# Kernel optimization log

Hardware: AMD Instinct MI355X
Metric: run time of the kernel (lower is better)

## Reference

```python
import jax, jax.numpy as jnp
import numpy as np

# Config (matches init_kwargs)
N_PARTS = 4
N_DATASETS = 2
N_VOLUMES = 16
N_TRANSFORMS = 2
TEMP_FAC = 0.1
BS = N_PARTS * N_DATASETS * N_VOLUMES          # 128
N_TOTAL = BS * (N_TRANSFORMS + 1)              # 384 rows in reg_pred
D_FEAT = 131072
PD = N_PARTS * N_DATASETS                      # class period for denominator exclusion
EPS = 1e-6


def setup_inputs() -> dict:
    key = jax.random.key(0)
    reg_pred = jax.random.normal(key, (N_TOTAL, D_FEAT), dtype=jnp.float32)
    return {"reg_pred": reg_pred}


def reference(reg_pred) -> jnp.ndarray:
    # Cosine similarity with torch's eps clamp on each norm.
    norms = jnp.maximum(jnp.linalg.norm(reg_pred, axis=1, keepdims=True), EPS)
    xn = reg_pred / norms                                   # [N, D]
    sims = (xn @ xn.T) / TEMP_FAC                           # [N, N] full cos-sim matrix
    e = jnp.exp(sims)

    # Denominator for pos_index p excludes every column j with j % PD == p % PD
    # (dataset_similar=False, within_dataset=False). Precompute per-class column sums.
    jmod = jnp.arange(N_TOTAL) % PD                          # [N]
    class_sum = jax.ops.segment_sum(e.T, jmod, num_segments=PD).T  # [N, PD]
    row_sum = jnp.sum(e, axis=1)                             # [N]

    p = jnp.arange(BS)
    rem = p % PD
    i1 = p
    i2 = BS + p
    i3 = (p + PD) % N_TOTAL
    i4 = (BS + p + PD) % N_TOTAL
    i5 = 2 * BS + p
    i6 = (2 * BS + p + PD) % N_TOTAL

    def pair_loss(a, b):
        en = e[a, b]                                         # exp(cos(xi,xj)/t), [BS]
        den_a = row_sum[a] - class_sum[a, rem]               # sum exp over den indexes
        den_b = row_sum[b] - class_sum[b, rem]
        return jnp.sum(-jnp.log(en / (en + den_a)) - jnp.log(en / (en + den_b)))

    total = (pair_loss(i1, i2) + pair_loss(i3, i4) + pair_loss(i1, i3)
             + pair_loss(i2, i4) + pair_loss(i5, i6) + pair_loss(i2, i5)
             + pair_loss(i4, i6))
    return total / (N_TRANSFORMS * 3 * BS)
```

## Files before the change

kernel.cpp:

```cpp
#include <hip/hip_runtime.h>
#include <hip/hip_bf16.h>

#define N_TOTAL 384
#define BS 128
#define PD 8
#define D_FEAT 131072
#define EPS 1e-6f

#define NSTRIP 256
#define COLS_PER (D_FEAT / NSTRIP)
#define CHUNK 64
#define NCH (COLS_PER / CHUNK)
#define NSWEEP 12
#define NSLOT 24

typedef __attribute__((ext_vector_type(4))) float f32x4;
typedef __attribute__((ext_vector_type(8))) __bf16 bf16x8;
typedef __attribute__((ext_vector_type(4))) __bf16 bf16x4;

typedef __attribute__((address_space(1))) const unsigned int gu32;
typedef __attribute__((address_space(3))) unsigned int lu32;

__device__ __forceinline__ void gload16(const void* g, void* l) {
    __builtin_amdgcn_global_load_lds((gu32*)g, (lu32*)l, 16, 0, 0);
}

static __device__ const int SAt[8][3] = {{0,0,0},{0,0,0},{1,1,1},{1,1,1},
                                         {2,2,4},{2,2,4},{3,3,5},{3,3,5}};
static __device__ const int SBt[8][3] = {{0,1,2},{3,4,5},{0,1,2},{3,4,5},
                                         {2,3,4},{4,5,5},{2,3,4},{4,5,5}};
static __device__ const int SRB2[NSLOT] = {0,0,0, 0,0,0, 1,1,1, 1,1,1,
                                           2,2,4, 2,2,4, 3,3,5, 3,3,5};
static __device__ const int SCB2[NSLOT] = {0,1,2, 3,4,5, 0,1,2, 3,4,5,
                                           2,3,4, 4,5,5, 2,3,4, 4,5,5};

__device__ __forceinline__ float gsym(const float* __restrict__ G, int i, int j) {
    return ((i >> 7) <= (j >> 7)) ? G[(size_t)i * N_TOTAL + j]
                                  : G[(size_t)j * N_TOTAL + i];
}

__device__ __forceinline__ bf16x8 fragb(const char* smb, int row, int ks, int kg) {
    return *(const bf16x8*)(smb + row * 128 + ((((ks << 2) | kg) ^ (row & 7)) << 4));
}

__global__ __launch_bounds__(512) void gram_fused_kernel(const float* __restrict__ X,
                                                         __bf16* __restrict__ P) {
    __shared__ char smf[N_TOTAL * 256];
    __shared__ char smb[N_TOTAL * 128];

    const int strip = blockIdx.x;
    const int tid  = threadIdx.x;
    const int wave = tid >> 6;
    const int lane = tid & 63;
    const int r16  = lane & 15;
    const int kg   = lane >> 4;

    const int A0 = SAt[wave][0] * 64, A2 = SAt[wave][2] * 64;
    const int B0 = SBt[wave][0] * 64, B1 = SBt[wave][1] * 64, B2 = SBt[wave][2] * 64;

    const char* src0 = (const char*)X + (size_t)(tid >> 4) * (D_FEAT * 4)
                     + (size_t)strip * (COLS_PER * 4) + (tid & 15) * 16;

    const int cr   = tid >> 4;
    const int g16  = tid & 15;
    const int wswz = ((((g16 >> 1) ^ (cr & 7)) << 4) | ((g16 & 1) << 3));

    f32x4 acc0[4][4], acc1[4][4], acc2[4][4];
#pragma unroll
    for (int m = 0; m < 4; m++)
#pragma unroll
        for (int n = 0; n < 4; n++) {
            acc0[m][n] = (f32x4)(0.0f); acc1[m][n] = (f32x4)(0.0f); acc2[m][n] = (f32x4)(0.0f);
        }

#define STAGE(t)                                                                          \
    _Pragma("unroll") for (int s = 0; s < NSWEEP; s++)                                    \
        gload16(src0 + (size_t)s * (32ull * D_FEAT * 4) + (size_t)(t) * 256,              \
                smf + s * 8192 + tid * 16);

#define SUBT(accX, Bb, ks)                                                                \
    do {                                                                                  \
        bf16x8 bf[4];                                                                     \
        _Pragma("unroll") for (int n = 0; n < 4; n++)                                     \
            bf[n] = fragb(smb, (Bb) + n * 16 + r16, ks, kg);                              \
        _Pragma("unroll") for (int m = 0; m < 4; m++)                                     \
            _Pragma("unroll") for (int n = 0; n < 4; n++)                                 \
                accX[m][n] = __builtin_amdgcn_mfma_f32_16x16x32_bf16(af[m], bf[n],        \
                                                                     accX[m][n], 0, 0, 0);\
    } while (0)

    STAGE(0);

    for (int t = 0; t < NCH; ++t) {
        asm volatile("s_waitcnt vmcnt(0)" ::: "memory");
        __builtin_amdgcn_sched_barrier(0);
        __builtin_amdgcn_s_barrier();
        __builtin_amdgcn_sched_barrier(0);

#pragma unroll
        for (int s = 0; s < NSWEEP; s++) {
            const f32x4 v = *(const f32x4*)(smf + s * 8192 + tid * 16);
            bf16x4 o;
            o[0] = (__bf16)v[0]; o[1] = (__bf16)v[1];
            o[2] = (__bf16)v[2]; o[3] = (__bf16)v[3];
            *(bf16x4*)(smb + (s * 32 + cr) * 128 + wswz) = o;
        }

        asm volatile("s_waitcnt lgkmcnt(0)" ::: "memory");
        __builtin_amdgcn_sched_barrier(0);
        __builtin_amdgcn_s_barrier();
        __builtin_amdgcn_sched_barrier(0);
        if (t + 1 < NCH) STAGE(t + 1);

#pragma unroll
        for (int ks = 0; ks < 2; ++ks) {
            bf16x8 af[4];
#pragma unroll
            for (int m = 0; m < 4; m++) af[m] = fragb(smb, A0 + m * 16 + r16, ks, kg);
            SUBT(acc0, B0, ks);
            SUBT(acc1, B1, ks);
#pragma unroll
            for (int m = 0; m < 4; m++) af[m] = fragb(smb, A2 + m * 16 + r16, ks, kg);
            SUBT(acc2, B2, ks);
        }
    }
#undef STAGE
#undef SUBT

    const int crow = (lane >> 4) * 4;
    const int ccol = lane & 15;
#define STOREP(accX, s)                                                                   \
    do {                                                                                  \
        __bf16* base = P + ((size_t)strip * NSLOT + wave * 3 + (s)) * 4096;               \
        _Pragma("unroll") for (int m = 0; m < 4; m++)                                     \
            _Pragma("unroll") for (int n = 0; n < 4; n++) {                               \
                bf16x4 v;                                                                 \
                v[0] = (__bf16)accX[m][n][0]; v[1] = (__bf16)accX[m][n][1];               \
                v[2] = (__bf16)accX[m][n][2]; v[3] = (__bf16)accX[m][n][3];               \
                *(bf16x4*)(base + (n * 16 + ccol) * 64 + m * 16 + crow) = v;              \
            }                                                                             \
    } while (0)
    STOREP(acc0, 0);
    STOREP(acc1, 1);
    STOREP(acc2, 2);
#undef STOREP
}

__global__ __launch_bounds__(128) void reduce_kernel(const __bf16* __restrict__ P,
                                                     float* __restrict__ G) {
    const int gidx = blockIdx.x * 128 + threadIdx.x;
    const int slot = gidx >> 11;
    const int pe   = (gidx & 2047) * 2;

    const unsigned* p = (const unsigned*)(P + (size_t)slot * 4096 + pe);
    const size_t stride = (size_t)NSLOT * 4096 / 2;
    float s0 = 0.0f, s1 = 0.0f;
#pragma unroll 16
    for (int strip = 0; strip < NSTRIP; ++strip) {
        const unsigned u = p[stride * strip];
        s0 += __uint_as_float(u << 16);
        s1 += __uint_as_float(u & 0xffff0000u);
    }

    const int rb  = SRB2[slot] * 64;
    const int cb  = SCB2[slot] * 64;
    const int col = pe >> 6;
    const int row = pe & 63;
    G[(size_t)(rb + row)     * N_TOTAL + cb + col] = s0;
    G[(size_t)(rb + row + 1) * N_TOTAL + cb + col] = s1;
}

__global__ __launch_bounds__(128) void den_kernel(const float* __restrict__ G,
                                                  float* __restrict__ den) {
    const int i = blockIdx.x;
    __shared__ float sInv[N_TOTAL];
    for (int j = threadIdx.x; j < N_TOTAL; j += 128) {
        const float n = sqrtf(G[(size_t)j * N_TOTAL + j]);
        sInv[j] = 1.0f / fmaxf(n, EPS);
    }
    __syncthreads();

    const float mi  = sInv[i] * 10.0f;
    const int   myc = i & 7;
    float s = 0.0f;
    for (int j = threadIdx.x; j < N_TOTAL; j += 128) {
        if ((j & 7) != myc)
            s += expf(gsym(G, i, j) * mi * sInv[j]);
    }
#pragma unroll
    for (int off = 32; off > 0; off >>= 1) s += __shfl_down(s, off, 64);
    __shared__ float partial[2];
    if ((threadIdx.x & 63) == 0) partial[threadIdx.x >> 6] = s;
    __syncthreads();
    if (threadIdx.x == 0) den[i] = partial[0] + partial[1];
}

__global__ __launch_bounds__(256) void loss_kernel(const float* __restrict__ G,
                                                   const float* __restrict__ den,
                                                   float* __restrict__ out) {
    __shared__ float sInv[N_TOTAL];
    for (int j = threadIdx.x; j < N_TOTAL; j += 256) {
        const float n = sqrtf(G[(size_t)j * N_TOTAL + j]);
        sInv[j] = 1.0f / fmaxf(n, EPS);
    }
    __syncthreads();

    float s = 0.0f;
    for (int idx = threadIdx.x; idx < 7 * BS; idx += 256) {
        const int p   = idx & (BS - 1);
        const int set = idx >> 7;
        int a, b;
        switch (set) {
            case 0:  a = p;                        b = BS + p;                      break;
            case 1:  a = (p + PD) % N_TOTAL;       b = (BS + p + PD) % N_TOTAL;     break;
            case 2:  a = p;                        b = (p + PD) % N_TOTAL;          break;
            case 3:  a = BS + p;                   b = (BS + p + PD) % N_TOTAL;     break;
            case 4:  a = 2 * BS + p;               b = (2 * BS + p + PD) % N_TOTAL; break;
            case 5:  a = BS + p;                   b = 2 * BS + p;                  break;
            default: a = (BS + p + PD) % N_TOTAL;  b = (2 * BS + p + PD) % N_TOTAL; break;
        }
        const float en = expf(gsym(G, a, b) * sInv[a] * sInv[b] * 10.0f);
        s += log1pf(den[a] / en) + log1pf(den[b] / en);
    }
#pragma unroll
    for (int off = 32; off > 0; off >>= 1) s += __shfl_down(s, off, 64);
    __shared__ float partial[4];
    if ((threadIdx.x & 63) == 0) partial[threadIdx.x >> 6] = s;
    __syncthreads();
    if (threadIdx.x == 0)
        out[0] = (partial[0] + partial[1] + partial[2] + partial[3]) / 768.0f;
}

extern "C" void kernel_launch(void* const* d_in, const int* in_sizes, int n_in,
                              void* d_out, int out_size, void* d_ws, size_t ws_size,
                              hipStream_t stream) {
    (void)in_sizes; (void)n_in; (void)out_size; (void)ws_size;
    const float* X   = (const float*)d_in[0];
    float*       out = (float*)d_out;
    float*       G   = (float*)d_ws;
    float*       den = G + (size_t)N_TOTAL * N_TOTAL;
    __bf16*      P   = (__bf16*)((char*)d_ws + (1u << 20));

    gram_fused_kernel<<<NSTRIP, 512, 0, stream>>>(X, P);
    reduce_kernel<<<384, 128, 0, stream>>>(P, G);
    den_kernel<<<N_TOTAL, 128, 0, stream>>>(G, den);
    loss_kernel<<<1, 256, 0, stream>>>(G, den, out);
}
```

Before: 71.41 us.

## Split strip reduction into two-stage tree with vectorized 16-byte loads

Replaces the single reduce kernel, in which each thread serially summed 256 strips with 4-byte loads, by two kernels. The first has each block sum 16 strips for one slot using 32-byte vector loads per thread and write float partials. The second sums the 16 partial groups and scatters the result into the Gram matrix. This aims to cut the long serial dependency chain and raise memory-level parallelism in the reduction. In exchange it adds an extra kernel launch and a round trip of fp32 partials through global memory.

```diff
diff --git a/kernel.cpp b/kernel.cpp
--- a/kernel.cpp
+++ b/kernel.cpp
@@ -15,6 +15,7 @@
 #define NSLOT 24
 
 typedef __attribute__((ext_vector_type(4))) float f32x4;
+typedef __attribute__((ext_vector_type(4))) unsigned u32x4;
 typedef __attribute__((ext_vector_type(8))) __bf16 bf16x8;
 typedef __attribute__((ext_vector_type(4))) __bf16 bf16x4;
 
@@ -146,28 +147,56 @@
 #undef STOREP
 }
 
-__global__ __launch_bounds__(128) void reduce_kernel(const __bf16* __restrict__ P,
-                                                     float* __restrict__ G) {
-    const int gidx = blockIdx.x * 128 + threadIdx.x;
-    const int slot = gidx >> 11;
-    const int pe   = (gidx & 2047) * 2;
-
-    const unsigned* p = (const unsigned*)(P + (size_t)slot * 4096 + pe);
-    const size_t stride = (size_t)NSLOT * 4096 / 2;
-    float s0 = 0.0f, s1 = 0.0f;
-#pragma unroll 16
-    for (int strip = 0; strip < NSTRIP; ++strip) {
-        const unsigned u = p[stride * strip];
-        s0 += __uint_as_float(u << 16);
-        s1 += __uint_as_float(u & 0xffff0000u);
-    }
-
-    const int rb  = SRB2[slot] * 64;
-    const int cb  = SCB2[slot] * 64;
-    const int col = pe >> 6;
-    const int row = pe & 63;
-    G[(size_t)(rb + row)     * N_TOTAL + cb + col] = s0;
-    G[(size_t)(rb + row + 1) * N_TOTAL + cb + col] = s1;
+__global__ __launch_bounds__(256) void reduce1_kernel(const __bf16* __restrict__ P,
+                                                      float* __restrict__ G16) {
+    const int b    = blockIdx.x;
+    const int slot = b >> 4;
+    const int sg   = b & 15;
+    const int t    = threadIdx.x;
+
+    float acc[16];
+#pragma unroll
+    for (int j = 0; j < 16; j++) acc[j] = 0.0f;
+
+    const __bf16* base = P + ((size_t)(sg * 16) * NSLOT + slot) * 4096 + t * 16;
+#pragma unroll
+    for (int s = 0; s < 16; s++) {
+        const u32x4* p = (const u32x4*)(base + (size_t)s * NSLOT * 4096);
+        const u32x4 v0 = p[0];
+        const u32x4 v1 = p[1];
+#pragma unroll
+        for (int k = 0; k < 4; k++) {
+            acc[2 * k]     += __uint_as_float(v0[k] << 16);
+            acc[2 * k + 1] += __uint_as_float(v0[k] & 0xffff0000u);
+            acc[8 + 2 * k] += __uint_as_float(v1[k] << 16);
+            acc[9 + 2 * k] += __uint_as_float(v1[k] & 0xffff0000u);
+        }
+    }
+
+    float* o = G16 + (size_t)b * 4096 + t * 16;
+#pragma unroll
+    for (int k = 0; k < 4; k++)
+        *(f32x4*)(o + 4 * k) = (f32x4){acc[4 * k], acc[4 * k + 1], acc[4 * k + 2], acc[4 * k + 3]};
+}
+
+__global__ __launch_bounds__(256) void reduce2_kernel(const float* __restrict__ G16,
+                                                      float* __restrict__ G) {
+    const int e    = (blockIdx.x * 256 + threadIdx.x) * 4;
+    const int slot = e >> 12;
+    const int el   = e & 4095;
+
+    f32x4 s = (f32x4)(0.0f);
+#pragma unroll
+    for (int g = 0; g < 16; g++)
+        s += *(const f32x4*)(G16 + ((size_t)(slot * 16 + g)) * 4096 + el);
+
+    const int rb = SRB2[slot] * 64;
+    const int cb = SCB2[slot] * 64;
+    const int col = el >> 6;
+    const int row = el & 63;
+#pragma unroll
+    for (int j = 0; j < 4; j++)
+        G[(size_t)(rb + row + j) * N_TOTAL + cb + col] = s[j];
 }
 
 __global__ __launch_bounds__(128) void den_kernel(const float* __restrict__ G,
@@ -240,9 +269,11 @@
     float*       G   = (float*)d_ws;
     float*       den = G + (size_t)N_TOTAL * N_TOTAL;
     __bf16*      P   = (__bf16*)((char*)d_ws + (1u << 20));
+    float*       G16 = (float*)((char*)d_ws + (56u << 20));
 
     gram_fused_kernel<<<NSTRIP, 512, 0, stream>>>(X, P);
-    reduce_kernel<<<384, 128, 0, stream>>>(P, G);
+    reduce1_kernel<<<384, 256, 0, stream>>>(P, G16);
+    reduce2_kernel<<<96, 256, 0, stream>>>(G16, G);
     den_kernel<<<N_TOTAL, 128, 0, stream>>>(G, den);
     loss_kernel<<<1, 256, 0, stream>>>(G, den, out);
 }
```

Result: slower. 74.50 us (+4.3%).
